# Optimization experiments

Hardware: AMD Instinct MI355X
Metric: run time of the kernel (lower is better)

Reference implementation:

```python
import jax, jax.numpy as jnp
import numpy as np
from jax import lax

B, CIN, H, W = 8, 256, 32, 32
DK, DV, NH = 256, 256, 8
DKH = DK // NH
COUT = 512  # output_dim; conv path has COUT - DV channels
KS, PAD = 3, 1


def setup_inputs() -> dict:
    key = jax.random.key(0)
    ks = jax.random.split(key, 9)
    scale = DKH ** (-0.5)
    return {
        "x": jax.random.normal(ks[0], (B, CIN, H, W), jnp.float32),
        "w_qkv": jax.random.normal(ks[1], (2 * DK + DV, CIN), jnp.float32) * 0.02,
        "b_qkv": jnp.zeros((2 * DK + DV,), jnp.float32),
        "w_attn": jax.random.normal(ks[2], (DV, DV), jnp.float32) * 0.02,
        "b_attn": jnp.zeros((DV,), jnp.float32),
        "w_out": jax.random.normal(ks[3], (COUT - DV, CIN, KS, KS), jnp.float32) * 0.02,
        "b_out": jnp.zeros((COUT - DV,), jnp.float32),
        # original: dkh**-0.5 + torch.rand(2*W-1, dkh)
        "key_rel_w": scale + jax.random.uniform(ks[4], (2 * W - 1, DKH), jnp.float32),
        "key_rel_h": scale + jax.random.uniform(ks[5], (2 * H - 1, DKH), jnp.float32),
    }


def _conv1x1(x, w, b):
    return jnp.einsum("bchw,oc->bohw", x, w) + b[None, :, None, None]


def _rel_to_abs(x):
    # x: [b, nh, L, 2L-1] -> [b, nh, L, L] via pad-reshape-slice trick
    b, nh, L, _ = x.shape
    x = jnp.pad(x, ((0, 0), (0, 0), (0, 0), (0, 1)))            # [b,nh,L,2L]
    flat = x.reshape(b, nh, L * 2 * L)
    flat = jnp.pad(flat, ((0, 0), (0, 0), (0, L - 1)))
    final = flat.reshape(b, nh, L + 1, 2 * L - 1)
    return final[:, :, :L, L - 1:]


def _rel_logits_1d(q5, rel_k, h, w, nh, perm):
    # q5: [b, nh, dkh, h, w]; rel_k: [2w-1, dkh]
    b = q5.shape[0]
    rel = jnp.einsum("bhdxy,md->bhxym", q5, rel_k)               # [b,nh,h,w,2w-1]
    rel = rel.reshape(b, nh * h, w, 2 * w - 1)
    rel = _rel_to_abs(rel)                                        # [b,nh*h,w,w]
    rel = rel.reshape(b, nh, h, w, w)
    rel = jnp.broadcast_to(rel[:, :, :, None], (b, nh, h, h, w, w))
    rel = jnp.transpose(rel, perm)                                # [b,nh,H,W,H,W]
    return rel.reshape(b, nh, h * w, h * w)


def reference(x, w_qkv, b_qkv, w_attn, b_attn, w_out, b_out, key_rel_w, key_rel_h):
    b = x.shape[0]
    hw = H * W
    # parallel conv path (3x3, pad 1)
    conv_out = lax.conv_general_dilated(
        x, w_out, window_strides=(1, 1), padding=((PAD, PAD), (PAD, PAD)),
        dimension_numbers=("NCHW", "OIHW", "NCHW")) + b_out[None, :, None, None]
    # qkv via 1x1 conv
    qkv = _conv1x1(x, w_qkv, b_qkv)
    q, k, v = jnp.split(qkv, [DK, 2 * DK], axis=1)
    q = q.reshape(b, NH, DKH, hw) * (DKH ** (-0.5))
    k = k.reshape(b, NH, DKH, hw)
    v = v.reshape(b, NH, DV // NH, hw)
    logits = jnp.einsum("bhdq,bhdk->bhqk", q, k)                  # [b,nh,HW,HW]
    q5 = q.reshape(b, NH, DKH, H, W)
    w_rel = _rel_logits_1d(q5, key_rel_w, H, W, NH, (0, 1, 2, 4, 3, 5))
    h_rel = _rel_logits_1d(jnp.transpose(q5, (0, 1, 2, 4, 3)), key_rel_h, W, H, NH,
                           (0, 1, 4, 2, 5, 3))
    logits = logits + h_rel + w_rel
    weights = jax.nn.softmax(logits, axis=-1)
    attn = jnp.einsum("bhqk,bhdk->bhdq", weights, v)              # [b,nh,dvh,HW]
    attn = attn.reshape(b, DV, H, W)
    attn = _conv1x1(attn, w_attn, b_attn)
    return jnp.concatenate([conv_out, attn], axis=1)
```

## Files before the change

kernel.cpp:

```cpp
#include <hip/hip_runtime.h>
#include <hip/hip_bf16.h>


typedef __hip_bfloat16 bf16;
using short8 = __attribute__((ext_vector_type(8))) short;
using short4v = __attribute__((ext_vector_type(4))) short;
using f32x4 = __attribute__((ext_vector_type(4))) float;

__device__ __forceinline__ short f2bs(float f) {
  union { bf16 b; short s; } u; u.b = __float2bfloat16(f); return u.s;
}
__device__ __forceinline__ float bs2f(short s) {
  union { unsigned u; float f; } x; x.u = ((unsigned)(unsigned short)s) << 16;
  return x.f;
}

__device__ __forceinline__ size_t wtile(int o, int c) {
  return ((size_t)((o >> 4) * 8 + (c >> 5)) * 512) +
         (((c >> 3) & 3) * 16 + (o & 15)) * 8 + (c & 7);
}

__global__ __launch_bounds__(256) void xpose(
    const float* __restrict__ X, short* __restrict__ xt,
    short* __restrict__ xb2) {
  const int b = blockIdx.x, r = blockIdx.y;
  const int tid = threadIdx.x;
  if (r == 0 || r == 33) {
    short8 z = {};
    short* dst = xt + (((size_t)b * 34 + r) * 34) * 256;
    for (int g = tid; g < 1088; g += 256) *(short8*)(dst + g * 8) = z;
    return;
  }
  __shared__ short xls[32][264];
  {
    const float* src = X + (size_t)b * 256 * 1024 + (r - 1) * 32;
    for (int it = 0; it < 8; ++it) {
      int idx = it * 256 + tid;
      int c = idx >> 3, pq = idx & 7;
      float4 f4 = *(const float4*)(src + (size_t)c * 1024 + pq * 4);
      xls[pq * 4 + 0][c] = f2bs(f4.x);
      xls[pq * 4 + 1][c] = f2bs(f4.y);
      xls[pq * 4 + 2][c] = f2bs(f4.z);
      xls[pq * 4 + 3][c] = f2bs(f4.w);
    }
  }
  __syncthreads();
  {
    short* dst = xt + (((size_t)b * 34 + r) * 34) * 256;
    for (int it = 0; it < 4; ++it) {
      int idx = it * 256 + tid;
      int cc = idx >> 5, co = idx & 31;
      short8 v = *(const short8*)&xls[cc][co * 8];
      *(short8*)(dst + (cc + 1) * 256 + co * 8) = v;
    }
    if (tid < 64) {
      short8 z = {};
      int cce = (tid >> 5) * 33, co = tid & 31;
      *(short8*)(dst + cce * 256 + co * 8) = z;
    }
  }
  {
    short* dst = xb2 + (((size_t)b * 64 + (r - 1) * 2) * 8) * 512;
    for (int it = 0; it < 4; ++it) {
      int g = it * 256 + tid;
      int half = g >> 9, c8 = (g >> 6) & 7, grp = (g >> 4) & 3, pcol = g & 15;
      short8 v = *(const short8*)&xls[half * 16 + pcol][c8 * 32 + grp * 8];
      *(short8*)(dst + ((half * 8 + c8) * 64 + grp * 16 + pcol) * 8) = v;
    }
  }
}

__global__ __launch_bounds__(256) void wpack(
    const float* __restrict__ Wc, short* __restrict__ Wb2,
    const float* __restrict__ wq, short* __restrict__ Wq2,
    const float* __restrict__ wa, short* __restrict__ Wa2) {
  const int bid = blockIdx.x;
  const int tid = threadIdx.x;
  if (bid < 256) {
    __shared__ float ws[2304];
    const float* src = Wc + (size_t)bid * 2304;
    for (int it = 0; it < 9; ++it) ws[it * 256 + tid] = src[it * 256 + tid];
    __syncthreads();
    const int o = bid, c = tid;
#pragma unroll
    for (int tap = 0; tap < 9; ++tap)
      Wb2[(size_t)tap * 65536 + wtile(o, c)] = f2bs(ws[c * 9 + tap]);
  } else if (bid < 1024) {
    const int o = bid - 256, c = tid;
    Wq2[wtile(o, c)] = f2bs(wq[o * 256 + c]);
  } else {
    const int o = bid - 1024, c = tid;
    Wa2[wtile(o, c)] = f2bs(wa[o * 256 + c]);
  }
}

__global__ __launch_bounds__(256) void qkv_mfma(
    const short* __restrict__ Wq2, const short* __restrict__ xb2,
    const float* __restrict__ bias,
    short* __restrict__ qsb, short* __restrict__ ksb2, short* __restrict__ vtb2) {
  const int tid = threadIdx.x;
  const int w = tid >> 6, lane = tid & 63;
  const int col = lane & 15, grp = lane >> 4;
  const int b = blockIdx.z;
  const int bx = blockIdx.x;
  const int p0 = bx * 64;
  const int ob = blockIdx.y * 128 + w * 16;
  const int o16 = ob >> 4;

  const short* wbase = Wq2 + lane * 8;
  const short* xpb = xb2 + (((size_t)b * 64 + bx * 4) * 8) * 512 + lane * 8;

  f32x4 acc[2][4] = {};
#pragma unroll
  for (int c8 = 0; c8 < 8; ++c8) {
    short8 a0 = *(const short8*)(wbase + (size_t)(o16 * 8 + c8) * 512);
    short8 a1 = *(const short8*)(wbase + (size_t)((o16 + 4) * 8 + c8) * 512);
    short8 b0 = *(const short8*)(xpb + c8 * 512);
    short8 b1 = *(const short8*)(xpb + 4096 + c8 * 512);
    short8 b2 = *(const short8*)(xpb + 8192 + c8 * 512);
    short8 b3 = *(const short8*)(xpb + 12288 + c8 * 512);
    acc[0][0] = __builtin_amdgcn_mfma_f32_16x16x32_bf16(a0, b0, acc[0][0], 0, 0, 0);
    acc[0][1] = __builtin_amdgcn_mfma_f32_16x16x32_bf16(a0, b1, acc[0][1], 0, 0, 0);
    acc[0][2] = __builtin_amdgcn_mfma_f32_16x16x32_bf16(a0, b2, acc[0][2], 0, 0, 0);
    acc[0][3] = __builtin_amdgcn_mfma_f32_16x16x32_bf16(a0, b3, acc[0][3], 0, 0, 0);
    acc[1][0] = __builtin_amdgcn_mfma_f32_16x16x32_bf16(a1, b0, acc[1][0], 0, 0, 0);
    acc[1][1] = __builtin_amdgcn_mfma_f32_16x16x32_bf16(a1, b1, acc[1][1], 0, 0, 0);
    acc[1][2] = __builtin_amdgcn_mfma_f32_16x16x32_bf16(a1, b2, acc[1][2], 0, 0, 0);
    acc[1][3] = __builtin_amdgcn_mfma_f32_16x16x32_bf16(a1, b3, acc[1][3], 0, 0, 0);
  }

  const float qscale = 0.17677669529663687f;
#pragma unroll
  for (int j = 0; j < 2; ++j) {
    const int obase = ob + j * 64 + grp * 4;
    const int sect = obase >> 8;
    const int nh = (obase >> 5) & 7;
    const int d0 = obase & 31;
    const size_t hb = ((size_t)(b * 8 + nh)) * 1024;
    const size_t hb2 = ((size_t)(b * 8 + nh)) * 32768;
    float bv[4];
#pragma unroll
    for (int r = 0; r < 4; ++r) bv[r] = bias[obase + r];
    if (sect == 0) {
#pragma unroll
      for (int pp = 0; pp < 4; ++pp) {
        const int p = p0 + pp * 16 + col;
        short4v o4;
#pragma unroll
        for (int r = 0; r < 4; ++r)
          o4[r] = f2bs((acc[j][pp][r] + bv[r]) * qscale);
        *(short4v*)&qsb[(hb + p) * 32 + d0] = o4;
      }
    } else if (sect == 1) {
      const size_t kb = hb2 + (size_t)bx * 2048 + (w & 1) * 256 +
                        (grp >> 1) * 128 + col * 8 + (grp & 1) * 4;
#pragma unroll
      for (int pp = 0; pp < 4; ++pp) {
        short4v o4;
#pragma unroll
        for (int r = 0; r < 4; ++r)
          o4[r] = f2bs(acc[j][pp][r] + bv[r]);
        *(short4v*)&ksb2[kb + pp * 512] = o4;
      }
    } else {
      const size_t vb0 = hb2 + (size_t)bx * 2048 + (size_t)(w & 1) * 512 +
                         (col >> 3) * 128 + (grp * 4) * 8 + (col & 7);
#pragma unroll
      for (int pp = 0; pp < 4; ++pp) {
        const size_t vb = vb0 + (pp >> 1) * 1024 + (pp & 1) * 256;
#pragma unroll
        for (int r = 0; r < 4; ++r)
          vtb2[vb + r * 8] = f2bs(acc[j][pp][r] + bv[r]);
      }
    }
  }
}

__global__ __launch_bounds__(256, 4) void attn_mfma(
    const short* __restrict__ qsb, const short* __restrict__ ksb2,
    const short* __restrict__ vtb2,
    const float* __restrict__ relw_g, const float* __restrict__ relh_g,
    short* __restrict__ amt2) {
  const int tid = threadIdx.x;
  const int w = tid >> 6, lane = tid & 63;
  const int col = lane & 15, grp = lane >> 4, g8 = grp * 8;
  const int qt = blockIdx.x * 4 + w;
  const int bnh = blockIdx.y;
  const int q0 = qt * 16;
  const int i = qt >> 1;
  const int j0 = (qt & 1) * 16;

  const short* Qb = qsb + (size_t)bnh * 32768;

  __shared__ short Gh_s[4][16][68];
  __shared__ short kvb[2][8][512];
  __shared__ short Pt_s[4][2][16][40];
  short* Gw_w = &Pt_s[w][0][0][0];

  const short* gK = ksb2 + (size_t)bnh * 32768 + w * 512 + lane * 8;
  const short* gV = vtb2 + (size_t)bnh * 32768 + w * 512 + lane * 8;

  short8 stgK = *(const short8*)gK;
  short8 stgV = *(const short8*)gV;

  short8 b_q = *(const short8*)(Qb + (q0 + col) * 32 + g8);

  {
    const float* rels[2] = {relh_g, relw_g};
#pragma unroll
    for (int tb = 0; tb < 2; ++tb) {
      const float* relg = rels[tb];
#pragma unroll
      for (int t = 0; t < 4; ++t) {
        int m = 16 * t + col;
        int mc = m > 62 ? 62 : m;
        const float* rp = relg + mc * 32 + g8;
        float4 f0 = *(const float4*)rp;
        float4 f1 = *(const float4*)(rp + 4);
        short8 ar;
        ar[0] = f2bs(f0.x); ar[1] = f2bs(f0.y);
        ar[2] = f2bs(f0.z); ar[3] = f2bs(f0.w);
        ar[4] = f2bs(f1.x); ar[5] = f2bs(f1.y);
        ar[6] = f2bs(f1.z); ar[7] = f2bs(f1.w);
        f32x4 d = __builtin_amdgcn_mfma_f32_16x16x32_bf16(
            ar, b_q, (f32x4){0.f, 0.f, 0.f, 0.f}, 0, 0, 0);
        short4v o;
        o[0] = f2bs(d[0]); o[1] = f2bs(d[1]);
        o[2] = f2bs(d[2]); o[3] = f2bs(d[3]);
        short* Gd = tb ? Gw_w : &Gh_s[w][0][0];
        *(short4v*)(Gd + col * 68 + 16 * t + grp * 4) = o;
      }
    }
  }
  __asm__ volatile("s_waitcnt lgkmcnt(0)" ::: "memory");

  float gw[8];
#pragma unroll
  for (int t = 0; t < 2; ++t)
#pragma unroll
    for (int r = 0; r < 4; ++r)
      gw[t * 4 + r] =
          bs2f(Gw_w[col * 68 + t * 16 + grp * 4 + r - j0 - col + 31]);

  const short8 a_one = {0x3F80, 0x3F80, 0x3F80, 0x3F80,
                        0x3F80, 0x3F80, 0x3F80, 0x3F80};

  f32x4 acc0 = {0.f, 0.f, 0.f, 0.f};
  f32x4 acc1 = {0.f, 0.f, 0.f, 0.f};
  f32x4 accl = {0.f, 0.f, 0.f, 0.f};

  short8 cvA0p = {}, cvA1p = {}, cvB0p = {}, cvB1p = {};

  *(short8*)&kvb[0][w][lane * 8] = stgK;
  *(short8*)&kvb[0][4 + w][lane * 8] = stgV;
  __syncthreads();

#pragma unroll 2
  for (int it = 0; it < 16; ++it) {
    const int cur = it & 1;
    if (it < 15) {
      stgK = *(const short8*)(gK + (size_t)(it + 1) * 2048);
      stgV = *(const short8*)(gV + (size_t)(it + 1) * 2048);
    }
    short8 ck0  = *(const short8*)&kvb[cur][0][lane * 8];
    short8 ck1  = *(const short8*)&kvb[cur][1][lane * 8];
    short8 ck2  = *(const short8*)&kvb[cur][2][lane * 8];
    short8 ck3  = *(const short8*)&kvb[cur][3][lane * 8];
    short8 cva0 = *(const short8*)&kvb[cur][4][lane * 8];
    short8 cva1 = *(const short8*)&kvb[cur][5][lane * 8];
    short8 cvb0 = *(const short8*)&kvb[cur][6][lane * 8];
    short8 cvb1 = *(const short8*)&kvb[cur][7][lane * 8];

    f32x4 s0 = __builtin_amdgcn_mfma_f32_16x16x32_bf16(
        ck0, b_q, (f32x4){0.f, 0.f, 0.f, 0.f}, 0, 0, 0);
    f32x4 s1 = __builtin_amdgcn_mfma_f32_16x16x32_bf16(
        ck1, b_q, (f32x4){0.f, 0.f, 0.f, 0.f}, 0, 0, 0);
    f32x4 s2 = __builtin_amdgcn_mfma_f32_16x16x32_bf16(
        ck2, b_q, (f32x4){0.f, 0.f, 0.f, 0.f}, 0, 0, 0);
    f32x4 s3 = __builtin_amdgcn_mfma_f32_16x16x32_bf16(
        ck3, b_q, (f32x4){0.f, 0.f, 0.f, 0.f}, 0, 0, 0);

    if (it > 0) {
      short8 pA = *(const short8*)&Pt_s[w][0][col][g8];
      short8 pB = *(const short8*)&Pt_s[w][1][col][g8];
      acc0 = __builtin_amdgcn_mfma_f32_16x16x32_bf16(cvA0p, pA, acc0, 0, 0, 0);
      acc0 = __builtin_amdgcn_mfma_f32_16x16x32_bf16(cvB0p, pB, acc0, 0, 0, 0);
      acc1 = __builtin_amdgcn_mfma_f32_16x16x32_bf16(cvA1p, pA, acc1, 0, 0, 0);
      acc1 = __builtin_amdgcn_mfma_f32_16x16x32_bf16(cvB1p, pB, acc1, 0, 0, 0);
      accl = __builtin_amdgcn_mfma_f32_16x16x32_bf16(a_one, pA, accl, 0, 0, 0);
      accl = __builtin_amdgcn_mfma_f32_16x16x32_bf16(a_one, pB, accl, 0, 0, 0);
    }

    float ghA = bs2f(Gh_s[w][col][2 * it - i + 31]);
    float ghB = bs2f(Gh_s[w][col][2 * it + 1 - i + 31]);
    short4v p0, p1, p2, p3;
#pragma unroll
    for (int r = 0; r < 4; ++r) p0[r] = f2bs(__expf(s0[r] + ghA + gw[r]));
#pragma unroll
    for (int r = 0; r < 4; ++r) p1[r] = f2bs(__expf(s1[r] + ghA + gw[4 + r]));
#pragma unroll
    for (int r = 0; r < 4; ++r) p2[r] = f2bs(__expf(s2[r] + ghB + gw[r]));
#pragma unroll
    for (int r = 0; r < 4; ++r) p3[r] = f2bs(__expf(s3[r] + ghB + gw[4 + r]));
    *(short4v*)&Pt_s[w][0][col][grp * 4] = p0;
    *(short4v*)&Pt_s[w][0][col][16 + grp * 4] = p1;
    *(short4v*)&Pt_s[w][1][col][grp * 4] = p2;
    *(short4v*)&Pt_s[w][1][col][16 + grp * 4] = p3;

    if (it < 15) {
      *(short8*)&kvb[cur ^ 1][w][lane * 8] = stgK;
      *(short8*)&kvb[cur ^ 1][4 + w][lane * 8] = stgV;
    }
    cvA0p = cva0; cvA1p = cva1; cvB0p = cvb0; cvB1p = cvb1;
    __syncthreads();
  }

  {
    short8 pA = *(const short8*)&Pt_s[w][0][col][g8];
    short8 pB = *(const short8*)&Pt_s[w][1][col][g8];
    acc0 = __builtin_amdgcn_mfma_f32_16x16x32_bf16(cvA0p, pA, acc0, 0, 0, 0);
    acc0 = __builtin_amdgcn_mfma_f32_16x16x32_bf16(cvB0p, pB, acc0, 0, 0, 0);
    acc1 = __builtin_amdgcn_mfma_f32_16x16x32_bf16(cvA1p, pA, acc1, 0, 0, 0);
    acc1 = __builtin_amdgcn_mfma_f32_16x16x32_bf16(cvB1p, pB, acc1, 0, 0, 0);
    accl = __builtin_amdgcn_mfma_f32_16x16x32_bf16(a_one, pA, accl, 0, 0, 0);
    accl = __builtin_amdgcn_mfma_f32_16x16x32_bf16(a_one, pB, accl, 0, 0, 0);
  }

  float rn = 1.0f / accl[0];
  const int bq = bnh >> 3, nh = bnh & 7;
  short* amb = amt2 + (((size_t)bq * 64 + qt) * 8 + nh) * 512 +
               (grp >> 1) * 128 + col * 8 + (grp & 1) * 4;
  short4v o4a, o4b;
#pragma unroll
  for (int r = 0; r < 4; ++r) {
    o4a[r] = f2bs(acc0[r] * rn);
    o4b[r] = f2bs(acc1[r] * rn);
  }
  *(short4v*)&amb[0] = o4a;
  *(short4v*)&amb[256] = o4b;
}

__global__ __launch_bounds__(256) void proj_mfma(
    const short* __restrict__ Wa2, const short* __restrict__ amt2,
    const float* __restrict__ bias, float* __restrict__ out) {
  const int tid = threadIdx.x;
  const int w = tid >> 6, lane = tid & 63;
  const int col = lane & 15, grp = lane >> 4;
  const int b = blockIdx.z;
  const int bx = blockIdx.x;
  const int p0 = bx * 64;
  const int ob = blockIdx.y * 128 + w * 16;
  const int o16 = ob >> 4;

  const short* wbase = Wa2 + lane * 8;
  const short* xpb = amt2 + (((size_t)b * 64 + bx * 4) * 8) * 512 + lane * 8;

  f32x4 acc[2][4] = {};
#pragma unroll
  for (int c8 = 0; c8 < 8; ++c8) {
    short8 a0 = *(const short8*)(wbase + (size_t)(o16 * 8 + c8) * 512);
    short8 a1 = *(const short8*)(wbase + (size_t)((o16 + 4) * 8 + c8) * 512);
    short8 b0 = *(const short8*)(xpb + c8 * 512);
    short8 b1 = *(const short8*)(xpb + 4096 + c8 * 512);
    short8 b2 = *(const short8*)(xpb + 8192 + c8 * 512);
    short8 b3 = *(const short8*)(xpb + 12288 + c8 * 512);
    acc[0][0] = __builtin_amdgcn_mfma_f32_16x16x32_bf16(a0, b0, acc[0][0], 0, 0, 0);
    acc[0][1] = __builtin_amdgcn_mfma_f32_16x16x32_bf16(a0, b1, acc[0][1], 0, 0, 0);
    acc[0][2] = __builtin_amdgcn_mfma_f32_16x16x32_bf16(a0, b2, acc[0][2], 0, 0, 0);
    acc[0][3] = __builtin_amdgcn_mfma_f32_16x16x32_bf16(a0, b3, acc[0][3], 0, 0, 0);
    acc[1][0] = __builtin_amdgcn_mfma_f32_16x16x32_bf16(a1, b0, acc[1][0], 0, 0, 0);
    acc[1][1] = __builtin_amdgcn_mfma_f32_16x16x32_bf16(a1, b1, acc[1][1], 0, 0, 0);
    acc[1][2] = __builtin_amdgcn_mfma_f32_16x16x32_bf16(a1, b2, acc[1][2], 0, 0, 0);
    acc[1][3] = __builtin_amdgcn_mfma_f32_16x16x32_bf16(a1, b3, acc[1][3], 0, 0, 0);
  }

#pragma unroll
  for (int j = 0; j < 2; ++j) {
    const int obase = ob + j * 64 + grp * 4;
    float bv[4];
#pragma unroll
    for (int r = 0; r < 4; ++r) bv[r] = bias[obase + r];
#pragma unroll
    for (int pp = 0; pp < 4; ++pp) {
      const int p = p0 + pp * 16 + col;
#pragma unroll
      for (int r = 0; r < 4; ++r)
        out[((size_t)b * 512 + 256 + obase + r) * 1024 + p] =
            acc[j][pp][r] + bv[r];
    }
  }
}

__global__ __launch_bounds__(256) void conv_mfma(
    const short* __restrict__ xt, const short* __restrict__ Wb2,
    const float* __restrict__ bias, float* __restrict__ out) {
  const int tid = threadIdx.x;
  const int w = tid >> 6, lane = tid & 63;
  const int col = lane & 15, grp = lane >> 4, g8 = grp * 8;
  const int r0 = blockIdx.x;
  const int oh = blockIdx.y;
  const int bb = blockIdx.z;

  __shared__ short xs[3][34][264];

  {
    const short* src = xt + (((size_t)bb * 34 + r0) * 34) * 256;
    for (int g = tid; g < 3264; g += 256) {
      int row = g / 1088;
      int rem = g - row * 1088;
      int cc = rem >> 5, chg = rem & 31;
      short8 v = *(const short8*)(src + (row * 34 + cc) * 256 + chg * 8);
      *(short8*)&xs[row][cc][chg * 8] = v;
    }
  }
  __syncthreads();

  const int ob0 = oh * 128 + w * 16;
  const int o16_0 = oh * 8 + w;
  const short* wbase = Wb2 + lane * 8;

  f32x4 acc00 = {0.f, 0.f, 0.f, 0.f};
  f32x4 acc01 = {0.f, 0.f, 0.f, 0.f};
  f32x4 acc10 = {0.f, 0.f, 0.f, 0.f};
  f32x4 acc11 = {0.f, 0.f, 0.f, 0.f};

#pragma unroll 1
  for (int tap = 0; tap < 9; ++tap) {
    const int u = (tap * 11) >> 5, v = tap - 3 * u;
    const short* wt = wbase + (size_t)tap * 65536;
    const short* xb0 = &xs[u][col + v][g8];
    const short* xb1 = &xs[u][col + 16 + v][g8];
#pragma unroll
    for (int c8 = 0; c8 < 8; ++c8) {
      const int chb = c8 * 32;
      short8 a0 = *(const short8*)(wt + (size_t)(o16_0 * 8 + c8) * 512);
      short8 a1 = *(const short8*)(wt + (size_t)((o16_0 + 4) * 8 + c8) * 512);
      short8 b0 = *(const short8*)(xb0 + chb);
      short8 b1 = *(const short8*)(xb1 + chb);
      acc00 = __builtin_amdgcn_mfma_f32_16x16x32_bf16(a0, b0, acc00, 0, 0, 0);
      acc01 = __builtin_amdgcn_mfma_f32_16x16x32_bf16(a0, b1, acc01, 0, 0, 0);
      acc10 = __builtin_amdgcn_mfma_f32_16x16x32_bf16(a1, b0, acc10, 0, 0, 0);
      acc11 = __builtin_amdgcn_mfma_f32_16x16x32_bf16(a1, b1, acc11, 0, 0, 0);
    }
  }

  const int ob1 = ob0 + 64;
  float* ob = out + (size_t)bb * 512 * 1024 + r0 * 32;
#pragma unroll
  for (int r = 0; r < 4; ++r) {
    int o0 = ob0 + grp * 4 + r;
    int o1 = ob1 + grp * 4 + r;
    float bv0 = bias[o0], bv1 = bias[o1];
    ob[(size_t)o0 * 1024 + col]      = acc00[r] + bv0;
    ob[(size_t)o0 * 1024 + 16 + col] = acc01[r] + bv0;
    ob[(size_t)o1 * 1024 + col]      = acc10[r] + bv1;
    ob[(size_t)o1 * 1024 + 16 + col] = acc11[r] + bv1;
  }
}

extern "C" void kernel_launch(void* const* d_in, const int* in_sizes, int n_in,
                              void* d_out, int out_size, void* d_ws, size_t ws_size,
                              hipStream_t stream) {
  const float* x      = (const float*)d_in[0];
  const float* w_qkv  = (const float*)d_in[1];
  const float* b_qkv  = (const float*)d_in[2];
  const float* w_attn = (const float*)d_in[3];
  const float* b_attn = (const float*)d_in[4];
  const float* w_out  = (const float*)d_in[5];
  const float* b_out  = (const float*)d_in[6];
  const float* relw   = (const float*)d_in[7];
  const float* relh   = (const float*)d_in[8];
  float* out = (float*)d_out;

  short* qsb  = (short*)d_ws;
  short* ksb2 = qsb + (size_t)2 * 1024 * 1024;
  short* vtb2 = ksb2 + (size_t)2 * 1024 * 1024;
  short* amt2 = (short*)((char*)d_ws + (size_t)12 * 1024 * 1024);
  short* xt   = (short*)((char*)d_ws + (size_t)16 * 1024 * 1024);
  short* xb2  = (short*)((char*)d_ws + (size_t)21 * 1024 * 1024);
  short* Wq2  = (short*)((char*)d_ws + (size_t)25 * 1024 * 1024);
  short* Wa2  = (short*)((char*)d_ws + (size_t)25 * 1024 * 1024 + 512 * 1024);
  short* Wb2  = (short*)((char*)d_ws + (size_t)26 * 1024 * 1024);

  xpose<<<dim3(8, 34), 256, 0, stream>>>(x, xt, xb2);
  wpack<<<1280, 256, 0, stream>>>(w_out, Wb2, w_qkv, Wq2, w_attn, Wa2);
  qkv_mfma<<<dim3(16, 6, 8), 256, 0, stream>>>(Wq2, xb2, b_qkv, qsb, ksb2, vtb2);
  attn_mfma<<<dim3(16, 64), 256, 0, stream>>>(qsb, ksb2, vtb2, relw, relh, amt2);
  proj_mfma<<<dim3(16, 2, 8), 256, 0, stream>>>(Wa2, amt2, b_attn, out);
  conv_mfma<<<dim3(32, 2, 8), 256, 0, stream>>>(xt, Wb2, b_out, out);
}
```

Before: 151.9 us.

## Merge prep and tail launches and fold log2e into q scale for exp2

Combines the input transpose and weight-packing kernels into a single `prep` launch, and the 3x3 conv and output projection kernels into a single `tail` launch, dispatching on block index. This cuts the launch count from six to four and lets conv and projection blocks share one grid. The attention softmax now uses raw `v_exp_f32` (exp2), with log2(e) folded into the q scaling constant. Because the relative-position logits are built from the same scaled q, they pick up the same factor. The risk is that all tail blocks now reserve the conv's large shared-memory buffer, including the projection blocks that do not use it.

```diff
diff --git a/kernel.cpp b/kernel.cpp
--- a/kernel.cpp
+++ b/kernel.cpp
@@ -14,83 +14,84 @@
   union { unsigned u; float f; } x; x.u = ((unsigned)(unsigned short)s) << 16;
   return x.f;
 }
+__device__ __forceinline__ float fexp2(float x) {
+  float r; asm("v_exp_f32 %0, %1" : "=v"(r) : "v"(x)); return r;
+}
 
 __device__ __forceinline__ size_t wtile(int o, int c) {
   return ((size_t)((o >> 4) * 8 + (c >> 5)) * 512) +
          (((c >> 3) & 3) * 16 + (o & 15)) * 8 + (c & 7);
 }
 
-__global__ __launch_bounds__(256) void xpose(
+__global__ __launch_bounds__(256) void prep(
     const float* __restrict__ X, short* __restrict__ xt,
-    short* __restrict__ xb2) {
-  const int b = blockIdx.x, r = blockIdx.y;
-  const int tid = threadIdx.x;
-  if (r == 0 || r == 33) {
-    short8 z = {};
-    short* dst = xt + (((size_t)b * 34 + r) * 34) * 256;
-    for (int g = tid; g < 1088; g += 256) *(short8*)(dst + g * 8) = z;
-    return;
-  }
-  __shared__ short xls[32][264];
-  {
-    const float* src = X + (size_t)b * 256 * 1024 + (r - 1) * 32;
-    for (int it = 0; it < 8; ++it) {
-      int idx = it * 256 + tid;
-      int c = idx >> 3, pq = idx & 7;
-      float4 f4 = *(const float4*)(src + (size_t)c * 1024 + pq * 4);
-      xls[pq * 4 + 0][c] = f2bs(f4.x);
-      xls[pq * 4 + 1][c] = f2bs(f4.y);
-      xls[pq * 4 + 2][c] = f2bs(f4.z);
-      xls[pq * 4 + 3][c] = f2bs(f4.w);
-    }
-  }
-  __syncthreads();
-  {
-    short* dst = xt + (((size_t)b * 34 + r) * 34) * 256;
-    for (int it = 0; it < 4; ++it) {
-      int idx = it * 256 + tid;
-      int cc = idx >> 5, co = idx & 31;
-      short8 v = *(const short8*)&xls[cc][co * 8];
-      *(short8*)(dst + (cc + 1) * 256 + co * 8) = v;
-    }
-    if (tid < 64) {
-      short8 z = {};
-      int cce = (tid >> 5) * 33, co = tid & 31;
-      *(short8*)(dst + cce * 256 + co * 8) = z;
-    }
-  }
-  {
-    short* dst = xb2 + (((size_t)b * 64 + (r - 1) * 2) * 8) * 512;
-    for (int it = 0; it < 4; ++it) {
-      int g = it * 256 + tid;
-      int half = g >> 9, c8 = (g >> 6) & 7, grp = (g >> 4) & 3, pcol = g & 15;
-      short8 v = *(const short8*)&xls[half * 16 + pcol][c8 * 32 + grp * 8];
-      *(short8*)(dst + ((half * 8 + c8) * 64 + grp * 16 + pcol) * 8) = v;
-    }
-  }
-}
-
-__global__ __launch_bounds__(256) void wpack(
+    short* __restrict__ xb2,
     const float* __restrict__ Wc, short* __restrict__ Wb2,
     const float* __restrict__ wq, short* __restrict__ Wq2,
     const float* __restrict__ wa, short* __restrict__ Wa2) {
+  __shared__ char smem[16896];
   const int bid = blockIdx.x;
   const int tid = threadIdx.x;
-  if (bid < 256) {
-    __shared__ float ws[2304];
-    const float* src = Wc + (size_t)bid * 2304;
+  if (bid < 272) {
+    const int b = bid / 34, r = bid - (bid / 34) * 34;
+    if (r == 0 || r == 33) {
+      short8 z = {};
+      short* dst = xt + (((size_t)b * 34 + r) * 34) * 256;
+      for (int g = tid; g < 1088; g += 256) *(short8*)(dst + g * 8) = z;
+      return;
+    }
+    short (*xls)[264] = (short(*)[264])smem;
+    {
+      const float* src = X + (size_t)b * 256 * 1024 + (r - 1) * 32;
+      for (int it = 0; it < 8; ++it) {
+        int idx = it * 256 + tid;
+        int c = idx >> 3, pq = idx & 7;
+        float4 f4 = *(const float4*)(src + (size_t)c * 1024 + pq * 4);
+        xls[pq * 4 + 0][c] = f2bs(f4.x);
+        xls[pq * 4 + 1][c] = f2bs(f4.y);
+        xls[pq * 4 + 2][c] = f2bs(f4.z);
+        xls[pq * 4 + 3][c] = f2bs(f4.w);
+      }
+    }
+    __syncthreads();
+    {
+      short* dst = xt + (((size_t)b * 34 + r) * 34) * 256;
+      for (int it = 0; it < 4; ++it) {
+        int idx = it * 256 + tid;
+        int cc = idx >> 5, co = idx & 31;
+        short8 v = *(const short8*)&xls[cc][co * 8];
+        *(short8*)(dst + (cc + 1) * 256 + co * 8) = v;
+      }
+      if (tid < 64) {
+        short8 z = {};
+        int cce = (tid >> 5) * 33, co = tid & 31;
+        *(short8*)(dst + cce * 256 + co * 8) = z;
+      }
+    }
+    {
+      short* dst = xb2 + (((size_t)b * 64 + (r - 1) * 2) * 8) * 512;
+      for (int it = 0; it < 4; ++it) {
+        int g = it * 256 + tid;
+        int half = g >> 9, c8 = (g >> 6) & 7, grp = (g >> 4) & 3, pcol = g & 15;
+        short8 v = *(const short8*)&xls[half * 16 + pcol][c8 * 32 + grp * 8];
+        *(short8*)(dst + ((half * 8 + c8) * 64 + grp * 16 + pcol) * 8) = v;
+      }
+    }
+  } else if (bid < 528) {
+    float* ws = (float*)smem;
+    const int o = bid - 272;
+    const float* src = Wc + (size_t)o * 2304;
     for (int it = 0; it < 9; ++it) ws[it * 256 + tid] = src[it * 256 + tid];
     __syncthreads();
-    const int o = bid, c = tid;
 #pragma unroll
     for (int tap = 0; tap < 9; ++tap)
-      Wb2[(size_t)tap * 65536 + wtile(o, c)] = f2bs(ws[c * 9 + tap]);
-  } else if (bid < 1024) {
-    const int o = bid - 256, c = tid;
-    Wq2[wtile(o, c)] = f2bs(wq[o * 256 + c]);
+      Wb2[(size_t)tap * 65536 + wtile(o, tid)] = f2bs(ws[tid * 9 + tap]);
+  } else if (bid < 1296) {
+    const int o = bid - 528;
+    Wq2[wtile(o, tid)] = f2bs(wq[o * 256 + tid]);
   } else {
-    const int o = bid - 1024, c = tid;
-    Wa2[wtile(o, c)] = f2bs(wa[o * 256 + c]);
+    const int o = bid - 1296;
+    Wa2[wtile(o, tid)] = f2bs(wa[o * 256 + tid]);
   }
 }
 
@@ -129,7 +130,7 @@
     acc[1][3] = __builtin_amdgcn_mfma_f32_16x16x32_bf16(a1, b3, acc[1][3], 0, 0, 0);
   }
 
-  const float qscale = 0.17677669529663687f;
+  const float qscale = 0.25503486f;
 #pragma unroll
   for (int j = 0; j < 2; ++j) {
     const int obase = ob + j * 64 + grp * 4;
@@ -295,13 +296,13 @@
     float ghB = bs2f(Gh_s[w][col][2 * it + 1 - i + 31]);
     short4v p0, p1, p2, p3;
 #pragma unroll
-    for (int r = 0; r < 4; ++r) p0[r] = f2bs(__expf(s0[r] + ghA + gw[r]));
-#pragma unroll
-    for (int r = 0; r < 4; ++r) p1[r] = f2bs(__expf(s1[r] + ghA + gw[4 + r]));
-#pragma unroll
-    for (int r = 0; r < 4; ++r) p2[r] = f2bs(__expf(s2[r] + ghB + gw[r]));
-#pragma unroll
-    for (int r = 0; r < 4; ++r) p3[r] = f2bs(__expf(s3[r] + ghB + gw[4 + r]));
+    for (int r = 0; r < 4; ++r) p0[r] = f2bs(fexp2(s0[r] + ghA + gw[r]));
+#pragma unroll
+    for (int r = 0; r < 4; ++r) p1[r] = f2bs(fexp2(s1[r] + ghA + gw[4 + r]));
+#pragma unroll
+    for (int r = 0; r < 4; ++r) p2[r] = f2bs(fexp2(s2[r] + ghB + gw[r]));
+#pragma unroll
+    for (int r = 0; r < 4; ++r) p3[r] = f2bs(fexp2(s3[r] + ghB + gw[4 + r]));
     *(short4v*)&Pt_s[w][0][col][grp * 4] = p0;
     *(short4v*)&Pt_s[w][0][col][16 + grp * 4] = p1;
     *(short4v*)&Pt_s[w][1][col][grp * 4] = p2;
@@ -340,121 +341,116 @@
   *(short4v*)&amb[256] = o4b;
 }
 
-__global__ __launch_bounds__(256) void proj_mfma(
+__global__ __launch_bounds__(256) void tail(
+    const short* __restrict__ xt, const short* __restrict__ Wb2,
+    const float* __restrict__ b_out,
     const short* __restrict__ Wa2, const short* __restrict__ amt2,
-    const float* __restrict__ bias, float* __restrict__ out) {
-  const int tid = threadIdx.x;
-  const int w = tid >> 6, lane = tid & 63;
-  const int col = lane & 15, grp = lane >> 4;
-  const int b = blockIdx.z;
-  const int bx = blockIdx.x;
-  const int p0 = bx * 64;
-  const int ob = blockIdx.y * 128 + w * 16;
-  const int o16 = ob >> 4;
-
-  const short* wbase = Wa2 + lane * 8;
-  const short* xpb = amt2 + (((size_t)b * 64 + bx * 4) * 8) * 512 + lane * 8;
-
-  f32x4 acc[2][4] = {};
-#pragma unroll
-  for (int c8 = 0; c8 < 8; ++c8) {
-    short8 a0 = *(const short8*)(wbase + (size_t)(o16 * 8 + c8) * 512);
-    short8 a1 = *(const short8*)(wbase + (size_t)((o16 + 4) * 8 + c8) * 512);
-    short8 b0 = *(const short8*)(xpb + c8 * 512);
-    short8 b1 = *(const short8*)(xpb + 4096 + c8 * 512);
-    short8 b2 = *(const short8*)(xpb + 8192 + c8 * 512);
-    short8 b3 = *(const short8*)(xpb + 12288 + c8 * 512);
-    acc[0][0] = __builtin_amdgcn_mfma_f32_16x16x32_bf16(a0, b0, acc[0][0], 0, 0, 0);
-    acc[0][1] = __builtin_amdgcn_mfma_f32_16x16x32_bf16(a0, b1, acc[0][1], 0, 0, 0);
-    acc[0][2] = __builtin_amdgcn_mfma_f32_16x16x32_bf16(a0, b2, acc[0][2], 0, 0, 0);
-    acc[0][3] = __builtin_amdgcn_mfma_f32_16x16x32_bf16(a0, b3, acc[0][3], 0, 0, 0);
-    acc[1][0] = __builtin_amdgcn_mfma_f32_16x16x32_bf16(a1, b0, acc[1][0], 0, 0, 0);
-    acc[1][1] = __builtin_amdgcn_mfma_f32_16x16x32_bf16(a1, b1, acc[1][1], 0, 0, 0);
-    acc[1][2] = __builtin_amdgcn_mfma_f32_16x16x32_bf16(a1, b2, acc[1][2], 0, 0, 0);
-    acc[1][3] = __builtin_amdgcn_mfma_f32_16x16x32_bf16(a1, b3, acc[1][3], 0, 0, 0);
-  }
-
-#pragma unroll
-  for (int j = 0; j < 2; ++j) {
-    const int obase = ob + j * 64 + grp * 4;
-    float bv[4];
-#pragma unroll
-    for (int r = 0; r < 4; ++r) bv[r] = bias[obase + r];
-#pragma unroll
-    for (int pp = 0; pp < 4; ++pp) {
-      const int p = p0 + pp * 16 + col;
-#pragma unroll
-      for (int r = 0; r < 4; ++r)
-        out[((size_t)b * 512 + 256 + obase + r) * 1024 + p] =
-            acc[j][pp][r] + bv[r];
-    }
-  }
-}
-
-__global__ __launch_bounds__(256) void conv_mfma(
-    const short* __restrict__ xt, const short* __restrict__ Wb2,
-    const float* __restrict__ bias, float* __restrict__ out) {
+    const float* __restrict__ b_attn, float* __restrict__ out) {
+  __shared__ short xs[3][34][264];
+  const int bid = blockIdx.x;
   const int tid = threadIdx.x;
   const int w = tid >> 6, lane = tid & 63;
   const int col = lane & 15, grp = lane >> 4, g8 = grp * 8;
-  const int r0 = blockIdx.x;
-  const int oh = blockIdx.y;
-  const int bb = blockIdx.z;
-
-  __shared__ short xs[3][34][264];
-
-  {
-    const short* src = xt + (((size_t)bb * 34 + r0) * 34) * 256;
-    for (int g = tid; g < 3264; g += 256) {
-      int row = g / 1088;
-      int rem = g - row * 1088;
-      int cc = rem >> 5, chg = rem & 31;
-      short8 v = *(const short8*)(src + (row * 34 + cc) * 256 + chg * 8);
-      *(short8*)&xs[row][cc][chg * 8] = v;
-    }
-  }
-  __syncthreads();
-
-  const int ob0 = oh * 128 + w * 16;
-  const int o16_0 = oh * 8 + w;
-  const short* wbase = Wb2 + lane * 8;
-
-  f32x4 acc00 = {0.f, 0.f, 0.f, 0.f};
-  f32x4 acc01 = {0.f, 0.f, 0.f, 0.f};
-  f32x4 acc10 = {0.f, 0.f, 0.f, 0.f};
-  f32x4 acc11 = {0.f, 0.f, 0.f, 0.f};
+
+  if (bid < 512) {
+    const int r0 = bid & 31, oh = (bid >> 5) & 1, bb = bid >> 6;
+    {
+      const short* src = xt + (((size_t)bb * 34 + r0) * 34) * 256;
+      for (int g = tid; g < 3264; g += 256) {
+        int row = g / 1088;
+        int rem = g - row * 1088;
+        int cc = rem >> 5, chg = rem & 31;
+        short8 v = *(const short8*)(src + (row * 34 + cc) * 256 + chg * 8);
+        *(short8*)&xs[row][cc][chg * 8] = v;
+      }
+    }
+    __syncthreads();
+
+    const int ob0 = oh * 128 + w * 16;
+    const int o16_0 = oh * 8 + w;
+    const short* wbase = Wb2 + lane * 8;
+
+    f32x4 acc00 = {0.f, 0.f, 0.f, 0.f};
+    f32x4 acc01 = {0.f, 0.f, 0.f, 0.f};
+    f32x4 acc10 = {0.f, 0.f, 0.f, 0.f};
+    f32x4 acc11 = {0.f, 0.f, 0.f, 0.f};
 
 #pragma unroll 1
-  for (int tap = 0; tap < 9; ++tap) {
-    const int u = (tap * 11) >> 5, v = tap - 3 * u;
-    const short* wt = wbase + (size_t)tap * 65536;
-    const short* xb0 = &xs[u][col + v][g8];
-    const short* xb1 = &xs[u][col + 16 + v][g8];
+    for (int tap = 0; tap < 9; ++tap) {
+      const int u = (tap * 11) >> 5, v = tap - 3 * u;
+      const short* wt = wbase + (size_t)tap * 65536;
+      const short* xb0 = &xs[u][col + v][g8];
+      const short* xb1 = &xs[u][col + 16 + v][g8];
+#pragma unroll
+      for (int c8 = 0; c8 < 8; ++c8) {
+        const int chb = c8 * 32;
+        short8 a0 = *(const short8*)(wt + (size_t)(o16_0 * 8 + c8) * 512);
+        short8 a1 = *(const short8*)(wt + (size_t)((o16_0 + 4) * 8 + c8) * 512);
+        short8 b0 = *(const short8*)(xb0 + chb);
+        short8 b1 = *(const short8*)(xb1 + chb);
+        acc00 = __builtin_amdgcn_mfma_f32_16x16x32_bf16(a0, b0, acc00, 0, 0, 0);
+        acc01 = __builtin_amdgcn_mfma_f32_16x16x32_bf16(a0, b1, acc01, 0, 0, 0);
+        acc10 = __builtin_amdgcn_mfma_f32_16x16x32_bf16(a1, b0, acc10, 0, 0, 0);
+        acc11 = __builtin_amdgcn_mfma_f32_16x16x32_bf16(a1, b1, acc11, 0, 0, 0);
+      }
+    }
+
+    const int ob1 = ob0 + 64;
+    float* ob = out + (size_t)bb * 512 * 1024 + r0 * 32;
+#pragma unroll
+    for (int r = 0; r < 4; ++r) {
+      int o0 = ob0 + grp * 4 + r;
+      int o1 = ob1 + grp * 4 + r;
+      float bv0 = b_out[o0], bv1 = b_out[o1];
+      ob[(size_t)o0 * 1024 + col]      = acc00[r] + bv0;
+      ob[(size_t)o0 * 1024 + 16 + col] = acc01[r] + bv0;
+      ob[(size_t)o1 * 1024 + col]      = acc10[r] + bv1;
+      ob[(size_t)o1 * 1024 + 16 + col] = acc11[r] + bv1;
+    }
+  } else {
+    const int t = bid - 512;
+    const int bx = t & 15, by = (t >> 4) & 1, b = t >> 5;
+    const int p0 = bx * 64;
+    const int ob = by * 128 + w * 16;
+    const int o16 = ob >> 4;
+
+    const short* wbase = Wa2 + lane * 8;
+    const short* xpb = amt2 + (((size_t)b * 64 + bx * 4) * 8) * 512 + lane * 8;
+
+    f32x4 acc[2][4] = {};
 #pragma unroll
     for (int c8 = 0; c8 < 8; ++c8) {
-      const int chb = c8 * 32;
-      short8 a0 = *(const short8*)(wt + (size_t)(o16_0 * 8 + c8) * 512);
-      short8 a1 = *(const short8*)(wt + (size_t)((o16_0 + 4) * 8 + c8) * 512);
-      short8 b0 = *(const short8*)(xb0 + chb);
-      short8 b1 = *(const short8*)(xb1 + chb);
-      acc00 = __builtin_amdgcn_mfma_f32_16x16x32_bf16(a0, b0, acc00, 0, 0, 0);
-      acc01 = __builtin_amdgcn_mfma_f32_16x16x32_bf16(a0, b1, acc01, 0, 0, 0);
-      acc10 = __builtin_amdgcn_mfma_f32_16x16x32_bf16(a1, b0, acc10, 0, 0, 0);
-      acc11 = __builtin_amdgcn_mfma_f32_16x16x32_bf16(a1, b1, acc11, 0, 0, 0);
-    }
-  }
-
-  const int ob1 = ob0 + 64;
-  float* ob = out + (size_t)bb * 512 * 1024 + r0 * 32;
-#pragma unroll
-  for (int r = 0; r < 4; ++r) {
-    int o0 = ob0 + grp * 4 + r;
-    int o1 = ob1 + grp * 4 + r;
-    float bv0 = bias[o0], bv1 = bias[o1];
-    ob[(size_t)o0 * 1024 + col]      = acc00[r] + bv0;
-    ob[(size_t)o0 * 1024 + 16 + col] = acc01[r] + bv0;
-    ob[(size_t)o1 * 1024 + col]      = acc10[r] + bv1;
-    ob[(size_t)o1 * 1024 + 16 + col] = acc11[r] + bv1;
+      short8 a0 = *(const short8*)(wbase + (size_t)(o16 * 8 + c8) * 512);
+      short8 a1 = *(const short8*)(wbase + (size_t)((o16 + 4) * 8 + c8) * 512);
+      short8 b0 = *(const short8*)(xpb + c8 * 512);
+      short8 b1 = *(const short8*)(xpb + 4096 + c8 * 512);
+      short8 b2 = *(const short8*)(xpb + 8192 + c8 * 512);
+      short8 b3 = *(const short8*)(xpb + 12288 + c8 * 512);
+      acc[0][0] = __builtin_amdgcn_mfma_f32_16x16x32_bf16(a0, b0, acc[0][0], 0, 0, 0);
+      acc[0][1] = __builtin_amdgcn_mfma_f32_16x16x32_bf16(a0, b1, acc[0][1], 0, 0, 0);
+      acc[0][2] = __builtin_amdgcn_mfma_f32_16x16x32_bf16(a0, b2, acc[0][2], 0, 0, 0);
+      acc[0][3] = __builtin_amdgcn_mfma_f32_16x16x32_bf16(a0, b3, acc[0][3], 0, 0, 0);
+      acc[1][0] = __builtin_amdgcn_mfma_f32_16x16x32_bf16(a1, b0, acc[1][0], 0, 0, 0);
+      acc[1][1] = __builtin_amdgcn_mfma_f32_16x16x32_bf16(a1, b1, acc[1][1], 0, 0, 0);
+      acc[1][2] = __builtin_amdgcn_mfma_f32_16x16x32_bf16(a1, b2, acc[1][2], 0, 0, 0);
+      acc[1][3] = __builtin_amdgcn_mfma_f32_16x16x32_bf16(a1, b3, acc[1][3], 0, 0, 0);
+    }
+
+#pragma unroll
+    for (int j = 0; j < 2; ++j) {
+      const int obase = ob + j * 64 + grp * 4;
+      float bv[4];
+#pragma unroll
+      for (int r = 0; r < 4; ++r) bv[r] = b_attn[obase + r];
+#pragma unroll
+      for (int pp = 0; pp < 4; ++pp) {
+        const int p = p0 + pp * 16 + col;
+#pragma unroll
+        for (int r = 0; r < 4; ++r)
+          out[((size_t)b * 512 + 256 + obase + r) * 1024 + p] =
+              acc[j][pp][r] + bv[r];
+      }
+    }
   }
 }
 
@@ -482,10 +478,9 @@
   short* Wa2  = (short*)((char*)d_ws + (size_t)25 * 1024 * 1024 + 512 * 1024);
   short* Wb2  = (short*)((char*)d_ws + (size_t)26 * 1024 * 1024);
 
-  xpose<<<dim3(8, 34), 256, 0, stream>>>(x, xt, xb2);
-  wpack<<<1280, 256, 0, stream>>>(w_out, Wb2, w_qkv, Wq2, w_attn, Wa2);
+  prep<<<1552, 256, 0, stream>>>(x, xt, xb2, w_out, Wb2, w_qkv, Wq2,
+                                 w_attn, Wa2);
   qkv_mfma<<<dim3(16, 6, 8), 256, 0, stream>>>(Wq2, xb2, b_qkv, qsb, ksb2, vtb2);
   attn_mfma<<<dim3(16, 64), 256, 0, stream>>>(qsb, ksb2, vtb2, relw, relh, amt2);
-  proj_mfma<<<dim3(16, 2, 8), 256, 0, stream>>>(Wa2, amt2, b_attn, out);
-  conv_mfma<<<dim3(32, 2, 8), 256, 0, stream>>>(xt, Wb2, b_out, out);
-}
+  tail<<<768, 256, 0, stream>>>(xt, Wb2, b_out, Wa2, amt2, b_attn, out);
+}
```

New measurement: 145.2 us. 1.05x faster.
